# Kernel optimization log

Measured on AMD Instinct MI355X. Metric: run time of the kernel, lower is better.

The kernel has to match this reference:

```python
import jax, jax.numpy as jnp
import numpy as np

S, B, H = 2048, 2, 2048
NH = 16
HD = H // NH  # 128
ROPE_BASE = 10000.0


def _rope_cos_sin(seq_len, dim, dtype):
    inv_freq = 1.0 / (ROPE_BASE ** (jnp.arange(0, dim, 2, dtype=jnp.float32) / dim))
    t = jnp.arange(seq_len, dtype=jnp.float32)
    freqs = jnp.outer(t, inv_freq)            # [S, dim/2]
    emb = jnp.concatenate([freqs, freqs], -1)  # [S, dim]
    return jnp.cos(emb).astype(dtype), jnp.sin(emb).astype(dtype)


def _rotate_half(x):
    x1, x2 = jnp.split(x, 2, axis=-1)
    return jnp.concatenate([-x2, x1], axis=-1)


def setup_inputs() -> dict:
    key = jax.random.key(0)
    k1, k2, k3 = jax.random.split(key, 3)
    hidden_states = jax.random.normal(k1, (S, B, H), dtype=jnp.float32)
    w_qkv = jax.random.normal(k2, (3 * H, H), dtype=jnp.float32) * (1.0 / np.sqrt(H))
    w_out = jax.random.normal(k3, (H, H), dtype=jnp.float32) * (1.0 / np.sqrt(H))
    return {"hidden_states": hidden_states, "w_qkv": w_qkv, "w_out": w_out}


def reference(hidden_states, w_qkv, w_out):
    seq_len, batch, _ = hidden_states.shape
    # QKV projection (nn.Linear: x @ W^T), bias=False
    qkv = jnp.einsum('sbh,oh->sbo', hidden_states, w_qkv)
    qkv = qkv.reshape(seq_len, batch, 3, NH, HD)
    q, k, v = qkv[:, :, 0], qkv[:, :, 1], qkv[:, :, 2]  # [S, B, NH, HD]

    cos, sin = _rope_cos_sin(seq_len, HD, hidden_states.dtype)
    cos = cos[:, None, None, :]
    sin = sin[:, None, None, :]
    q = q * cos + _rotate_half(q) * sin
    k = k * cos + _rotate_half(k) * sin

    # [S, B, NH, HD] -> [B, NH, S, HD]
    q = q.transpose(1, 2, 0, 3)
    k = k.transpose(1, 2, 0, 3)
    v = v.transpose(1, 2, 0, 3)

    scale = 1.0 / np.sqrt(HD)
    scores = jnp.einsum('bhqd,bhkd->bhqk', q, k) * scale
    causal = jnp.tril(jnp.ones((seq_len, seq_len), dtype=bool))
    scores = jnp.where(causal, scores, jnp.finfo(scores.dtype).min)
    probs = jax.nn.softmax(scores, axis=-1)
    attn = jnp.einsum('bhqk,bhkd->bhqd', probs, v)  # [B, NH, S, HD]

    # [B, NH, S, HD] -> [S, B, NH*HD]
    out = attn.transpose(2, 0, 1, 3).reshape(seq_len, batch, -1)
    out = jnp.einsum('sbh,oh->sbo', out, w_out)
    return out
```

## Files before the change

kernel.cpp:

```cpp
#include <hip/hip_runtime.h>
#include <hip/hip_bf16.h>

typedef __attribute__((ext_vector_type(8))) short bf16x8;
typedef __attribute__((ext_vector_type(8))) short s16x8;
typedef __attribute__((ext_vector_type(4))) float f32x4;
typedef __attribute__((ext_vector_type(4))) int i32x4;

#define SEQ 2048
#define BATCH 2
#define HID 2048
#define NH 16
#define HD 128
#define QKVN 6144

static __device__ __forceinline__ short f2bf(float f) {
    union { float f; unsigned u; } v; v.f = f;
    unsigned r = (v.u + 0x7FFFu + ((v.u >> 16) & 1u)) >> 16;
    return (short)r;
}

static __device__ __forceinline__ void gload_lds16(const short* g, short* l) {
    __builtin_amdgcn_global_load_lds((const __attribute__((address_space(1))) void*)g,
                                     (__attribute__((address_space(3))) void*)l, 16, 0, 0);
}

__global__ void cvt_kernel(const float* __restrict__ in, short* __restrict__ out, int n8) {
    const int i = blockIdx.x * 256 + threadIdx.x;
    if (i >= n8) return;
    f32x4 a = *(const f32x4*)(in + (size_t)i * 8);
    f32x4 b = *(const f32x4*)(in + (size_t)i * 8 + 4);
    s16x8 o = { f2bf(a.x), f2bf(a.y), f2bf(a.z), f2bf(a.w),
                f2bf(b.x), f2bf(b.y), f2bf(b.z), f2bf(b.w) };
    *(s16x8*)(out + (size_t)i * 8) = o;
}

template<bool STORE_BF16>
__global__ __launch_bounds__(256, 2)
void gemm_bt(const short* __restrict__ A, const short* __restrict__ B,
             void* __restrict__ Cp, int N, int K) {
    __shared__ short As[128 * 32];
    __shared__ short Bs[128 * 32];

    const int tid = threadIdx.x;
    const int mBase = blockIdx.y * 128;
    const int nBase = blockIdx.x * 128;
    const int w = tid >> 6, lane = tid & 63, quad = lane >> 4, l15 = lane & 15;
    const int wr = (w >> 1) * 64, wc = (w & 1) * 64;

    const int r0 = tid >> 2;
    const int kc = (tid & 3) * 8;
    const short* aG = A + (size_t)(mBase + r0) * K + kc;
    const short* bG = B + (size_t)(nBase + r0) * K + kc;
    short* ldsA0 = As + w * 512;
    short* ldsA1 = As + 2048 + w * 512;
    short* ldsB0 = Bs + w * 512;
    short* ldsB1 = Bs + 2048 + w * 512;

    f32x4 acc[4][4] = {};

    for (int k0 = 0; k0 < K; k0 += 32) {
        __syncthreads();
        gload_lds16(aG + k0,                    ldsA0);
        gload_lds16(aG + (size_t)64 * K + k0,   ldsA1);
        gload_lds16(bG + k0,                    ldsB0);
        gload_lds16(bG + (size_t)64 * K + k0,   ldsB1);
        __syncthreads();

        bf16x8 af[4], bfb[4];
        #pragma unroll
        for (int i = 0; i < 4; ++i)
            af[i] = *(const bf16x8*)(As + (wr + i * 16 + l15) * 32 + quad * 8);
        #pragma unroll
        for (int j = 0; j < 4; ++j)
            bfb[j] = *(const bf16x8*)(Bs + (wc + j * 16 + l15) * 32 + quad * 8);
        #pragma unroll
        for (int i = 0; i < 4; ++i)
            #pragma unroll
            for (int j = 0; j < 4; ++j)
                acc[i][j] = __builtin_amdgcn_mfma_f32_16x16x32_bf16(af[i], bfb[j], acc[i][j], 0, 0, 0);
    }

    #pragma unroll
    for (int i = 0; i < 4; ++i) {
        const int row0 = mBase + wr + i * 16 + quad * 4;
        #pragma unroll
        for (int j = 0; j < 4; ++j) {
            const int col = nBase + wc + j * 16 + l15;
            #pragma unroll
            for (int r = 0; r < 4; ++r) {
                if (STORE_BF16)
                    ((short*)Cp)[(size_t)(row0 + r) * N + col] = f2bf(acc[i][j][r]);
                else
                    ((float*)Cp)[(size_t)(row0 + r) * N + col] = acc[i][j][r];
            }
        }
    }
}

__global__ void rope_kernel(short* __restrict__ qkv) {
    const int tid = blockIdx.x * 256 + threadIdx.x;
    const int d     = tid & 63;
    const int h     = (tid >> 6) & 15;
    const int which = (tid >> 10) & 1;
    const int b     = (tid >> 11) & 1;
    const int s     = tid >> 12;

    const size_t base = (size_t)(s * 2 + b) * QKVN + which * 2048 + h * 128;
    const float inv_freq = expf(-((float)(2 * d) * (1.0f / 128.0f)) * 9.210340371976184f);
    float sn, cs;
    sincosf((float)s * inv_freq, &sn, &cs);
    const float post = (which == 0) ? 0.08838834764831845f : 1.0f;

    union { unsigned u; float f; } x1, x2;
    x1.u = ((unsigned)(unsigned short)qkv[base + d]) << 16;
    x2.u = ((unsigned)(unsigned short)qkv[base + d + 64]) << 16;
    qkv[base + d]      = f2bf((x1.f * cs - x2.f * sn) * post);
    qkv[base + d + 64] = f2bf((x2.f * cs + x1.f * sn) * post);
}

__global__ void vtrans_kernel(const short* __restrict__ qkv, short* __restrict__ vT) {
    __shared__ short T[64][72];
    const int s0 = blockIdx.x * 64, d0 = blockIdx.y * 64;
    const int bh = blockIdx.z;
    const int b = bh >> 4, h = bh & 15;
    const int t = threadIdx.x;

    #pragma unroll
    for (int p = 0; p < 2; ++p) {
        const int sl = (t >> 3) + p * 32;
        const int dl = (t & 7) * 8;
        *(i32x4*)&T[sl][dl] =
            *(const i32x4*)(qkv + (size_t)((s0 + sl) * 2 + b) * QKVN + 4096 + h * 128 + d0 + dl);
    }
    __syncthreads();
    #pragma unroll
    for (int p = 0; p < 2; ++p) {
        const int dl = (t >> 3) + p * 32;
        const int sl = (t & 7) * 8;
        short tmp[8];
        #pragma unroll
        for (int j = 0; j < 8; ++j) tmp[j] = T[sl + j][dl];
        *(i32x4*)(vT + ((size_t)bh * 128 + d0 + dl) * 2048 + s0 + sl) = *(i32x4*)tmp;
    }
}

__global__ __launch_bounds__(256, 2)
void attn_kernel(const short* __restrict__ qkv, const short* __restrict__ vT,
                 short* __restrict__ out) {
    __shared__ short Kt[64][136];
    __shared__ short Vt[128][72];
    __shared__ short Ps[4][32][72];

    const int bx = blockIdx.x;
    const int h = blockIdx.y, b = blockIdx.z;
    const int Aq = (bx & 1) ? (bx >> 1) : (15 - (bx >> 1));
    const int qt = b ? (15 - Aq) : Aq;
    const int tid = threadIdx.x;
    const int w = tid >> 6, lane = tid & 63, quad = lane >> 4, l15 = lane & 15;

    bf16x8 aq[2][4];
    #pragma unroll
    for (int m = 0; m < 2; ++m) {
        const short* qbase =
            qkv + (size_t)((qt * 128 + w * 32 + m * 16 + l15) * 2 + b) * QKVN + h * 128;
        #pragma unroll
        for (int c = 0; c < 4; ++c)
            aq[m][c] = *(const bf16x8*)(qbase + c * 32 + quad * 8);
    }

    f32x4 oacc[2][8] = {};
    float lpart[2][4] = {};

    const int kRow = tid >> 2, kCol = (tid & 3) * 32;
    const int vRow = tid >> 1, vCol = (tid & 1) * 32;
    const short* kG = qkv + (size_t)b * QKVN + 2048 + h * 128 + kCol;
    const short* vG = vT + ((size_t)(b * 16 + h) * 128 + vRow) * 2048 + vCol;

    const int nChunks = 2 * qt + 2;

    for (int ck = 0; ck < nChunks; ++ck) {
        const int kk0 = ck * 64;
        __syncthreads();
        {
            const short* kp = kG + (size_t)(kk0 + kRow) * 2 * QKVN;
            const short* vp = vG + kk0;
            i32x4 kv[4], vv[4];
            #pragma unroll
            for (int i = 0; i < 4; ++i) kv[i] = *(const i32x4*)(kp + i * 8);
            #pragma unroll
            for (int i = 0; i < 4; ++i) vv[i] = *(const i32x4*)(vp + i * 8);
            #pragma unroll
            for (int i = 0; i < 4; ++i) *(i32x4*)&Kt[kRow][kCol + i * 8] = kv[i];
            #pragma unroll
            for (int i = 0; i < 4; ++i) *(i32x4*)&Vt[vRow][vCol + i * 8] = vv[i];
        }
        __syncthreads();

        f32x4 sc4[2][4] = {};
        #pragma unroll
        for (int c = 0; c < 4; ++c) {
            #pragma unroll
            for (int n = 0; n < 4; ++n) {
                bf16x8 bk = *(const bf16x8*)&Kt[n * 16 + l15][c * 32 + quad * 8];
                #pragma unroll
                for (int m = 0; m < 2; ++m)
                    sc4[m][n] = __builtin_amdgcn_mfma_f32_16x16x32_bf16(aq[m][c], bk, sc4[m][n], 0, 0, 0);
            }
        }

        const bool diag = (ck >= 2 * qt);
        #pragma unroll
        for (int m = 0; m < 2; ++m) {
            const int rowbase = qt * 128 + w * 32 + m * 16 + quad * 4;
            #pragma unroll
            for (int r = 0; r < 4; ++r) {
                #pragma unroll
                for (int n = 0; n < 4; ++n) {
                    float sv = sc4[m][n][r];
                    if (diag && (kk0 + n * 16 + l15 > rowbase + r)) sv = -1e30f;
                    const float p = __expf(sv);
                    lpart[m][r] += p;
                    Ps[w][m * 16 + quad * 4 + r][n * 16 + l15] = f2bf(p);
                }
            }
        }

        #pragma unroll
        for (int m = 0; m < 2; ++m) {
            #pragma unroll
            for (int kp2 = 0; kp2 < 2; ++kp2) {
                bf16x8 ap = *(const bf16x8*)&Ps[w][m * 16 + l15][kp2 * 32 + quad * 8];
                #pragma unroll
                for (int dt = 0; dt < 8; ++dt) {
                    bf16x8 bv = *(const bf16x8*)&Vt[dt * 16 + l15][kp2 * 32 + quad * 8];
                    oacc[m][dt] = __builtin_amdgcn_mfma_f32_16x16x32_bf16(ap, bv, oacc[m][dt], 0, 0, 0);
                }
            }
        }
    }

    #pragma unroll
    for (int m = 0; m < 2; ++m) {
        const int rowbase = qt * 128 + w * 32 + m * 16 + quad * 4;
        #pragma unroll
        for (int r = 0; r < 4; ++r) {
            float l = lpart[m][r];
            #pragma unroll
            for (int off = 1; off < 16; off <<= 1)
                l += __shfl_xor(l, off);
            const float inv_l = 1.0f / l;
            const size_t obase = (size_t)((rowbase + r) * 2 + b) * HID + h * 128;
            #pragma unroll
            for (int dt = 0; dt < 8; ++dt)
                out[obase + dt * 16 + l15] = f2bf(oacc[m][dt][r] * inv_l);
        }
    }
}

extern "C" void kernel_launch(void* const* d_in, const int* in_sizes, int n_in,
                              void* d_out, int out_size, void* d_ws, size_t ws_size,
                              hipStream_t stream) {
    const float* hidden = (const float*)d_in[0];
    const float* w_qkv  = (const float*)d_in[1];
    const float* w_out  = (const float*)d_in[2];
    float* out = (float*)d_out;

    short* qkv     = (short*)d_ws;
    short* attnb   = qkv + (size_t)4096 * QKVN;
    short* wqkv_bf = attnb + (size_t)4096 * HID;
    short* wout_bf = wqkv_bf;
    short* hbf     = wqkv_bf + (size_t)QKVN * HID;
    short* vT      = hbf;

    dim3 blk(256);
    cvt_kernel<<<dim3(4096), blk, 0, stream>>>(hidden, hbf, 4096 * 256);
    cvt_kernel<<<dim3(6144), blk, 0, stream>>>(w_qkv, wqkv_bf, 6144 * 256);
    gemm_bt<true><<<dim3(QKVN / 128, 4096 / 128), blk, 0, stream>>>(
        hbf, wqkv_bf, qkv, QKVN, HID);
    cvt_kernel<<<dim3(2048), blk, 0, stream>>>(w_out, wout_bf, 2048 * 256);
    rope_kernel<<<dim3((SEQ * BATCH * 2 * NH * (HD / 2)) / 256), blk, 0, stream>>>(qkv);
    vtrans_kernel<<<dim3(SEQ / 64, HD / 64, BATCH * NH), blk, 0, stream>>>(qkv, vT);
    attn_kernel<<<dim3(SEQ / 128, NH, BATCH), blk, 0, stream>>>(qkv, vT, attnb);
    gemm_bt<false><<<dim3(HID / 128, 4096 / 128), blk, 0, stream>>>(
        attnb, wout_bf, out, HID, HID);
}
```

Measured before the change: 418.6 us.

## Add 256x256-tile 8-wave pipelined GEMM for QKV projection

Replaces the 128x128 tile QKV GEMM with a new 256x256 tile kernel using 512 threads. It double-buffers LDS with direct global-to-LDS loads, XOR-swizzles the LDS layout to avoid bank conflicts, and interleaves staging with MFMA quadrants under priority hints. The aim is more operand reuse per byte loaded and better overlap of memory and compute in the largest GEMM. The cost is heavy register and LDS use (128KB of LDS per block), and the 384 blocks may fill the device unevenly.

```diff
diff --git a/kernel.cpp b/kernel.cpp
--- a/kernel.cpp
+++ b/kernel.cpp
@@ -32,6 +32,137 @@
     s16x8 o = { f2bf(a.x), f2bf(a.y), f2bf(a.z), f2bf(a.w),
                 f2bf(b.x), f2bf(b.y), f2bf(b.z), f2bf(b.w) };
     *(s16x8*)(out + (size_t)i * 8) = o;
+}
+
+#define STAGE_A(BUF, H, KK) do { \
+    const short* _s = aSrc + (size_t)(H) * 64 * K + (KK) * 64; \
+    short* _d = lds + (BUF) * 16384 + (H) * 8192 + w * 512; \
+    gload_lds16(_s, _d); \
+    gload_lds16(_s + (size_t)128 * K, _d + 4096); \
+} while (0)
+
+#define STAGE_B(BUF, H, KK) do { \
+    const short* _s = bSrc + (size_t)(H) * 32 * K + (KK) * 64; \
+    short* _d = lds + 32768 + (BUF) * 16384 + (H) * 8192 + w * 512; \
+    gload_lds16(_s, _d); \
+    gload_lds16(_s + (size_t)128 * K, _d + 4096); \
+} while (0)
+
+#define LOAD_A(MH) do { \
+    const short* _p = lds + bufR * 16384 + (MH) * 8192 + aOff0; \
+    const short* _q = lds + bufR * 16384 + (MH) * 8192 + aOff1; \
+    _Pragma("unroll") \
+    for (int mm = 0; mm < 4; ++mm) { \
+        aR[mm][0] = *(const bf16x8*)(_p + mm * 1024); \
+        aR[mm][1] = *(const bf16x8*)(_q + mm * 1024); \
+    } \
+} while (0)
+
+#define LOAD_B(NHh) do { \
+    const short* _p = lds + 32768 + bufR * 16384 + (NHh) * 8192 + bOff0; \
+    const short* _q = lds + 32768 + bufR * 16384 + (NHh) * 8192 + bOff1; \
+    _Pragma("unroll") \
+    for (int nn = 0; nn < 2; ++nn) { \
+        bR[(NHh) * 2 + nn][0] = *(const bf16x8*)(_p + nn * 1024); \
+        bR[(NHh) * 2 + nn][1] = *(const bf16x8*)(_q + nn * 1024); \
+    } \
+} while (0)
+
+#define MFMA_Q(MH, NHh) do { \
+    _Pragma("unroll") \
+    for (int mm = 0; mm < 4; ++mm) { \
+        _Pragma("unroll") \
+        for (int nn = 0; nn < 2; ++nn) { \
+            f32x4 _c = acc[(MH) * 4 + mm][(NHh) * 2 + nn]; \
+            _c = __builtin_amdgcn_mfma_f32_16x16x32_bf16(aR[mm][0], bR[(NHh) * 2 + nn][0], _c, 0, 0, 0); \
+            _c = __builtin_amdgcn_mfma_f32_16x16x32_bf16(aR[mm][1], bR[(NHh) * 2 + nn][1], _c, 0, 0, 0); \
+            acc[(MH) * 4 + mm][(NHh) * 2 + nn] = _c; \
+        } \
+    } \
+} while (0)
+
+__global__ __launch_bounds__(512, 2)
+void gemm256(const short* __restrict__ A, const short* __restrict__ B,
+             short* __restrict__ C, int N, int K) {
+    __shared__ short lds[65536];
+
+    const int tid = threadIdx.x;
+    const int mBase = blockIdx.y * 256;
+    const int nBase = blockIdx.x * 256;
+    const int w = tid >> 6, lane = tid & 63, quad = lane >> 4, l15 = lane & 15;
+    const int wm = w >> 2, wn = w & 3;
+
+    const int kcol = 8 * ((tid & 7) ^ ((tid >> 3) & 7));
+    const short* aSrc = A + (size_t)(mBase + (tid >> 3)) * K + kcol;
+    const short* bSrc = B + (size_t)(nBase + ((tid >> 3) & 31) + ((tid >> 8) & 1) * 64) * K + kcol;
+
+    const int cs0 = (quad * 8) ^ ((l15 & 7) << 3);
+    const int aOff0 = (l15 + wm * 64) * 64 + cs0;
+    const int aOff1 = aOff0 ^ 32;
+    const int bOff0 = (l15 + wn * 32) * 64 + cs0;
+    const int bOff1 = bOff0 ^ 32;
+
+    const int NK = K >> 6;
+    f32x4 acc[8][4] = {};
+    bf16x8 aR[4][2], bR[4][2];
+
+    STAGE_A(0, 0, 0); STAGE_B(0, 0, 0); STAGE_B(0, 1, 0); STAGE_A(0, 1, 0);
+    STAGE_A(1, 0, 1); STAGE_B(1, 0, 1); STAGE_B(1, 1, 1);
+    asm volatile("s_waitcnt vmcnt(6)" ::: "memory");
+    __builtin_amdgcn_s_barrier();
+
+    int bufR = 0;
+    for (int k = 0; k < NK; ++k) {
+        const int kk1 = (k + 1 < NK) ? k + 1 : NK - 1;
+        const int kk2 = (k + 2 < NK) ? k + 2 : NK - 1;
+        LOAD_A(0);
+        LOAD_B(0);
+        STAGE_A(bufR ^ 1, 1, kk1);
+        asm volatile("s_waitcnt lgkmcnt(8)" ::: "memory");
+        __builtin_amdgcn_s_barrier();
+        asm volatile("s_waitcnt lgkmcnt(0)" ::: "memory");
+        __builtin_amdgcn_s_setprio(1);
+        MFMA_Q(0, 0);
+        __builtin_amdgcn_s_setprio(0);
+        __builtin_amdgcn_s_barrier();
+        LOAD_B(1);
+        STAGE_A(bufR, 0, kk2);
+        __builtin_amdgcn_s_barrier();
+        asm volatile("s_waitcnt lgkmcnt(0)" ::: "memory");
+        __builtin_amdgcn_s_setprio(1);
+        MFMA_Q(0, 1);
+        __builtin_amdgcn_s_setprio(0);
+        __builtin_amdgcn_s_barrier();
+        LOAD_A(1);
+        STAGE_B(bufR, 0, kk2);
+        __builtin_amdgcn_s_barrier();
+        asm volatile("s_waitcnt lgkmcnt(0)" ::: "memory");
+        __builtin_amdgcn_s_setprio(1);
+        MFMA_Q(1, 1);
+        __builtin_amdgcn_s_setprio(0);
+        __builtin_amdgcn_s_barrier();
+        STAGE_B(bufR, 1, kk2);
+        asm volatile("s_waitcnt vmcnt(6)" ::: "memory");
+        __builtin_amdgcn_s_barrier();
+        __builtin_amdgcn_s_setprio(1);
+        MFMA_Q(1, 0);
+        __builtin_amdgcn_s_setprio(0);
+        __builtin_amdgcn_s_barrier();
+        bufR ^= 1;
+    }
+    asm volatile("s_waitcnt vmcnt(0)" ::: "memory");
+
+    #pragma unroll
+    for (int f = 0; f < 8; ++f) {
+        const int row0 = mBase + wm * 128 + f * 16 + quad * 4;
+        #pragma unroll
+        for (int g = 0; g < 4; ++g) {
+            const int col = nBase + wn * 64 + g * 16 + l15;
+            #pragma unroll
+            for (int r = 0; r < 4; ++r)
+                C[(size_t)(row0 + r) * N + col] = f2bf(acc[f][g][r]);
+        }
+    }
 }
 
 template<bool STORE_BF16>
@@ -275,7 +406,7 @@
     dim3 blk(256);
     cvt_kernel<<<dim3(4096), blk, 0, stream>>>(hidden, hbf, 4096 * 256);
     cvt_kernel<<<dim3(6144), blk, 0, stream>>>(w_qkv, wqkv_bf, 6144 * 256);
-    gemm_bt<true><<<dim3(QKVN / 128, 4096 / 128), blk, 0, stream>>>(
+    gemm256<<<dim3(QKVN / 256, 4096 / 256), dim3(512), 0, stream>>>(
         hbf, wqkv_bf, qkv, QKVN, HID);
     cvt_kernel<<<dim3(2048), blk, 0, stream>>>(w_out, wout_bf, 2048 * 256);
     rope_kernel<<<dim3((SEQ * BATCH * 2 * NH * (HD / 2)) / 256), blk, 0, stream>>>(qkv);
```

After: 400.4 us. 1.05x faster.
